# Performance work log

Measured on AMD Instinct MI355X. Metric: run time of the kernel, lower is better.

The kernel has to match this reference:

```python
import jax, jax.numpy as jnp
import numpy as np

B, N = 128, 1024


def setup_inputs() -> dict:
    key = jax.random.key(0)
    k1, k2 = jax.random.split(key)
    vector = jax.random.uniform(k1, (B, N), dtype=jnp.float32)
    interactions = jax.random.normal(k2, (N, N), dtype=jnp.float32)
    return {"vector": vector, "interactions": interactions}


def reference(vector, interactions):
    # x: [B,1,N], y: [B,N,1] -> broadcast dirac delta [B,N,N]
    x = vector[:, None, :]
    y = vector[:, :, None]
    dd = (1.0 - x) * (1.0 - y) + x * y  # [B,N,N]
    dd = jnp.triu(dd)                   # keep upper triangle incl. diagonal
    energy = dd * interactions          # [B,N,N] * [N,N] broadcast
    return energy.reshape(vector.shape[0], -1).sum(axis=1)  # [B]
```

## Files before the change

### kernel.cpp

```cpp
#include <hip/hip_runtime.h>
#include <math.h>

#define NDIM 1024
#define BDIM 128
#define TS 32
#define NT (NDIM / TS)
#define NTILES (NT * (NT + 1) / 2)

__global__ __launch_bounds__(256) void potts_fused(
    const float* __restrict__ V,
    const float* __restrict__ W,
    float* __restrict__ out)
{
    const int t = blockIdx.x;
    const int u = NTILES - 1 - t;
    int kk = (int)(0.5f * (sqrtf((float)(8 * u + 1)) - 1.0f));
    if (kk * (kk + 1) / 2 > u) --kk;
    if ((kk + 1) * (kk + 2) / 2 <= u) ++kk;
    const int ti = NT - 1 - kk;
    const int tj = NT - 1 - (u - kk * (kk + 1) / 2);
    const int I0 = ti * TS, J0 = tj * TS;
    const bool diag = (ti == tj);

    __shared__ float4 vj4[BDIM][8];
    __shared__ float4 vi4[BDIM][8];
    __shared__ float rs[TS];
    __shared__ float red[4][BDIM];

    const int tid = threadIdx.x;
    const int w = tid >> 6;
    const int l = tid & 63;
    const int l7 = l & 7;

    {
        const int r = tid >> 3, c4 = (tid & 7) * 4;
        float4 w4 = *(const float4*)(W + (size_t)(I0 + r) * NDIM + (J0 + c4));
        if (diag) {
            if (c4 + 0 < r) w4.x = 0.0f;
            if (c4 + 1 < r) w4.y = 0.0f;
            if (c4 + 2 < r) w4.z = 0.0f;
            if (c4 + 3 < r) w4.w = 0.0f;
        }
        float rsum = (w4.x + w4.y) + (w4.z + w4.w);
        rsum += __shfl_xor(rsum, 1);
        rsum += __shfl_xor(rsum, 2);
        rsum += __shfl_xor(rsum, 4);
        if ((tid & 7) == 0) rs[r] = rsum;
    }

#pragma unroll
    for (int it = 0; it < 4; ++it) {
        const int fid = tid + 256 * it;
        const int b = fid >> 3, j4 = fid & 7;
        const int g = j4 ^ (b & 7);
        vj4[b][g] = *(const float4*)(V + (size_t)b * NDIM + (J0 + 4 * j4));
        vi4[b][g] = *(const float4*)(V + (size_t)b * NDIM + (I0 + 4 * j4));
    }
    __syncthreads();

    float vj0[TS], vj1[TS];
#pragma unroll
    for (int j4 = 0; j4 < 8; ++j4) {
        const int g = j4 ^ l7;
        const float4 a = vj4[l][g];
        vj0[4*j4+0] = a.x; vj0[4*j4+1] = a.y;
        vj0[4*j4+2] = a.z; vj0[4*j4+3] = a.w;
        const float4 c = vj4[l + 64][g];
        vj1[4*j4+0] = c.x; vj1[4*j4+1] = c.y;
        vj1[4*j4+2] = c.z; vj1[4*j4+3] = c.w;
    }
    float vi0[8], vi1[8];
    {
        const int ga = (2 * w) ^ l7, gb = (2 * w + 1) ^ l7;
        const float4 p  = vi4[l][ga],      q  = vi4[l][gb];
        const float4 p1 = vi4[l + 64][ga], q1 = vi4[l + 64][gb];
        vi0[0]=p.x;  vi0[1]=p.y;  vi0[2]=p.z;  vi0[3]=p.w;
        vi0[4]=q.x;  vi0[5]=q.y;  vi0[6]=q.z;  vi0[7]=q.w;
        vi1[0]=p1.x; vi1[1]=p1.y; vi1[2]=p1.z; vi1[3]=p1.w;
        vi1[4]=q1.x; vi1[5]=q1.y; vi1[6]=q1.z; vi1[7]=q1.w;
    }

    float acc0 = 0.0f, acc1 = 0.0f;
#pragma unroll
    for (int k = 0; k < 8; ++k) {
        const int i = 8 * w + k;
        const float* __restrict__ wrow = W + (size_t)(I0 + i) * NDIM + J0;
        float za0 = 0.f, zb0 = 0.f, za1 = 0.f, zb1 = 0.f;
#pragma unroll
        for (int j4 = 0; j4 < 8; j4 += 2) {
            float4 wa = *(const float4*)(wrow + 4 * j4);
            float4 wb = *(const float4*)(wrow + 4 * j4 + 4);
            if (diag) {
                if (4*j4 + 0 < i) wa.x = 0.0f;
                if (4*j4 + 1 < i) wa.y = 0.0f;
                if (4*j4 + 2 < i) wa.z = 0.0f;
                if (4*j4 + 3 < i) wa.w = 0.0f;
                if (4*j4 + 4 < i) wb.x = 0.0f;
                if (4*j4 + 5 < i) wb.y = 0.0f;
                if (4*j4 + 6 < i) wb.z = 0.0f;
                if (4*j4 + 7 < i) wb.w = 0.0f;
            }
            za0 = fmaf(wa.x, vj0[4*j4+0], za0);
            za0 = fmaf(wa.y, vj0[4*j4+1], za0);
            za0 = fmaf(wa.z, vj0[4*j4+2], za0);
            za0 = fmaf(wa.w, vj0[4*j4+3], za0);
            za1 = fmaf(wa.x, vj1[4*j4+0], za1);
            za1 = fmaf(wa.y, vj1[4*j4+1], za1);
            za1 = fmaf(wa.z, vj1[4*j4+2], za1);
            za1 = fmaf(wa.w, vj1[4*j4+3], za1);
            zb0 = fmaf(wb.x, vj0[4*j4+4], zb0);
            zb0 = fmaf(wb.y, vj0[4*j4+5], zb0);
            zb0 = fmaf(wb.z, vj0[4*j4+6], zb0);
            zb0 = fmaf(wb.w, vj0[4*j4+7], zb0);
            zb1 = fmaf(wb.x, vj1[4*j4+4], zb1);
            zb1 = fmaf(wb.y, vj1[4*j4+5], zb1);
            zb1 = fmaf(wb.z, vj1[4*j4+6], zb1);
            zb1 = fmaf(wb.w, vj1[4*j4+7], zb1);
        }
        const float y0 = vi0[k], y1 = vi1[k];
        const float rsk = rs[i];
        acc0 = fmaf(1.0f - y0, rsk, acc0);
        acc0 = fmaf(2.0f * y0 - 1.0f, za0 + zb0, acc0);
        acc1 = fmaf(1.0f - y1, rsk, acc1);
        acc1 = fmaf(2.0f * y1 - 1.0f, za1 + zb1, acc1);
    }

    red[w][l] = acc0;
    red[w][l + 64] = acc1;
    __syncthreads();
    if (tid < BDIM) {
        const float v4 = (red[0][tid] + red[1][tid]) + (red[2][tid] + red[3][tid]);
        atomicAdd(&out[tid], v4);
    }
}

extern "C" void kernel_launch(void* const* d_in, const int* in_sizes, int n_in,
                              void* d_out, int out_size, void* d_ws, size_t ws_size,
                              hipStream_t stream) {
    const float* V = (const float*)d_in[0];
    const float* W = (const float*)d_in[1];
    float* out = (float*)d_out;
    (void)d_ws; (void)ws_size;

    hipMemsetAsync(d_out, 0, BDIM * sizeof(float), stream);
    potts_fused<<<dim3(NTILES), dim3(256), 0, stream>>>(V, W, out);
}
```

Before: 77.46 us.

## Replace atomic accumulation with per-tile partials and a separate reduction kernel

The main kernel now writes each tile's per-batch sum to a workspace buffer instead of using atomicAdd, and a second kernel reduces the 528 partials per batch row. This also removes the output memset. The V row-slice loads for the i side now go straight from global memory into registers instead of through shared memory, and all global loads are issued up front so their latency overlaps. The cost is an extra kernel launch and a workspace round trip, in exchange for no atomic contention and less shared memory.

```diff
diff --git a/kernel.cpp b/kernel.cpp
--- a/kernel.cpp
+++ b/kernel.cpp
@@ -7,10 +7,10 @@
 #define NT (NDIM / TS)
 #define NTILES (NT * (NT + 1) / 2)
 
-__global__ __launch_bounds__(256) void potts_fused(
+__global__ __launch_bounds__(256) void potts_main(
     const float* __restrict__ V,
     const float* __restrict__ W,
-    float* __restrict__ out)
+    float* __restrict__ partial)
 {
     const int t = blockIdx.x;
     const int u = NTILES - 1 - t;
@@ -23,7 +23,6 @@
     const bool diag = (ti == tj);
 
     __shared__ float4 vj4[BDIM][8];
-    __shared__ float4 vi4[BDIM][8];
     __shared__ float rs[TS];
     __shared__ float red[4][BDIM];
 
@@ -32,15 +31,26 @@
     const int l = tid & 63;
     const int l7 = l & 7;
 
+    const int r = tid >> 3, c4 = (tid & 7) * 4;
+    float4 w4 = *(const float4*)(W + (size_t)(I0 + r) * NDIM + (J0 + c4));
+
+    float4 sv0 = *(const float4*)(V + (size_t)((tid + 0 * 256) >> 3) * NDIM + (J0 + 4 * ((tid + 0 * 256) & 7)));
+    float4 sv1 = *(const float4*)(V + (size_t)((tid + 1 * 256) >> 3) * NDIM + (J0 + 4 * ((tid + 1 * 256) & 7)));
+    float4 sv2 = *(const float4*)(V + (size_t)((tid + 2 * 256) >> 3) * NDIM + (J0 + 4 * ((tid + 2 * 256) & 7)));
+    float4 sv3 = *(const float4*)(V + (size_t)((tid + 3 * 256) >> 3) * NDIM + (J0 + 4 * ((tid + 3 * 256) & 7)));
+
+    const float4 p0 = *(const float4*)(V + (size_t)l * NDIM + (I0 + 8 * w));
+    const float4 q0 = *(const float4*)(V + (size_t)l * NDIM + (I0 + 8 * w + 4));
+    const float4 p1 = *(const float4*)(V + (size_t)(l + 64) * NDIM + (I0 + 8 * w));
+    const float4 q1 = *(const float4*)(V + (size_t)(l + 64) * NDIM + (I0 + 8 * w + 4));
+
+    if (diag) {
+        if (c4 + 0 < r) w4.x = 0.0f;
+        if (c4 + 1 < r) w4.y = 0.0f;
+        if (c4 + 2 < r) w4.z = 0.0f;
+        if (c4 + 3 < r) w4.w = 0.0f;
+    }
     {
-        const int r = tid >> 3, c4 = (tid & 7) * 4;
-        float4 w4 = *(const float4*)(W + (size_t)(I0 + r) * NDIM + (J0 + c4));
-        if (diag) {
-            if (c4 + 0 < r) w4.x = 0.0f;
-            if (c4 + 1 < r) w4.y = 0.0f;
-            if (c4 + 2 < r) w4.z = 0.0f;
-            if (c4 + 3 < r) w4.w = 0.0f;
-        }
         float rsum = (w4.x + w4.y) + (w4.z + w4.w);
         rsum += __shfl_xor(rsum, 1);
         rsum += __shfl_xor(rsum, 2);
@@ -48,13 +58,12 @@
         if ((tid & 7) == 0) rs[r] = rsum;
     }
 
-#pragma unroll
-    for (int it = 0; it < 4; ++it) {
-        const int fid = tid + 256 * it;
-        const int b = fid >> 3, j4 = fid & 7;
-        const int g = j4 ^ (b & 7);
-        vj4[b][g] = *(const float4*)(V + (size_t)b * NDIM + (J0 + 4 * j4));
-        vi4[b][g] = *(const float4*)(V + (size_t)b * NDIM + (I0 + 4 * j4));
+    {
+        int fid, b, j4;
+        fid = tid + 0 * 256; b = fid >> 3; j4 = fid & 7; vj4[b][j4 ^ (b & 7)] = sv0;
+        fid = tid + 1 * 256; b = fid >> 3; j4 = fid & 7; vj4[b][j4 ^ (b & 7)] = sv1;
+        fid = tid + 2 * 256; b = fid >> 3; j4 = fid & 7; vj4[b][j4 ^ (b & 7)] = sv2;
+        fid = tid + 3 * 256; b = fid >> 3; j4 = fid & 7; vj4[b][j4 ^ (b & 7)] = sv3;
     }
     __syncthreads();
 
@@ -70,15 +79,10 @@
         vj1[4*j4+2] = c.z; vj1[4*j4+3] = c.w;
     }
     float vi0[8], vi1[8];
-    {
-        const int ga = (2 * w) ^ l7, gb = (2 * w + 1) ^ l7;
-        const float4 p  = vi4[l][ga],      q  = vi4[l][gb];
-        const float4 p1 = vi4[l + 64][ga], q1 = vi4[l + 64][gb];
-        vi0[0]=p.x;  vi0[1]=p.y;  vi0[2]=p.z;  vi0[3]=p.w;
-        vi0[4]=q.x;  vi0[5]=q.y;  vi0[6]=q.z;  vi0[7]=q.w;
-        vi1[0]=p1.x; vi1[1]=p1.y; vi1[2]=p1.z; vi1[3]=p1.w;
-        vi1[4]=q1.x; vi1[5]=q1.y; vi1[6]=q1.z; vi1[7]=q1.w;
-    }
+    vi0[0]=p0.x; vi0[1]=p0.y; vi0[2]=p0.z; vi0[3]=p0.w;
+    vi0[4]=q0.x; vi0[5]=q0.y; vi0[6]=q0.z; vi0[7]=q0.w;
+    vi1[0]=p1.x; vi1[1]=p1.y; vi1[2]=p1.z; vi1[3]=p1.w;
+    vi1[4]=q1.x; vi1[5]=q1.y; vi1[6]=q1.z; vi1[7]=q1.w;
 
     float acc0 = 0.0f, acc1 = 0.0f;
 #pragma unroll
@@ -129,9 +133,26 @@
     red[w][l + 64] = acc1;
     __syncthreads();
     if (tid < BDIM) {
-        const float v4 = (red[0][tid] + red[1][tid]) + (red[2][tid] + red[3][tid]);
-        atomicAdd(&out[tid], v4);
+        partial[(size_t)tid * NTILES + t] =
+            (red[0][tid] + red[1][tid]) + (red[2][tid] + red[3][tid]);
     }
+}
+
+__global__ __launch_bounds__(256) void potts_red(
+    const float* __restrict__ partial, float* __restrict__ out)
+{
+    const int b = blockIdx.x;
+    const int tid = threadIdx.x;
+    const float* __restrict__ row = partial + (size_t)b * NTILES;
+    float a = row[tid] + row[tid + 256];
+    if (tid < NTILES - 512) a += row[tid + 512];
+#pragma unroll
+    for (int off = 32; off > 0; off >>= 1)
+        a += __shfl_down(a, off);
+    __shared__ float rr[4];
+    if ((tid & 63) == 0) rr[tid >> 6] = a;
+    __syncthreads();
+    if (tid == 0) out[b] = (rr[0] + rr[1]) + (rr[2] + rr[3]);
 }
 
 extern "C" void kernel_launch(void* const* d_in, const int* in_sizes, int n_in,
@@ -140,8 +161,8 @@
     const float* V = (const float*)d_in[0];
     const float* W = (const float*)d_in[1];
     float* out = (float*)d_out;
-    (void)d_ws; (void)ws_size;
+    float* partial = (float*)d_ws;
 
-    hipMemsetAsync(d_out, 0, BDIM * sizeof(float), stream);
-    potts_fused<<<dim3(NTILES), dim3(256), 0, stream>>>(V, W, out);
+    potts_main<<<dim3(NTILES), dim3(256), 0, stream>>>(V, W, partial);
+    potts_red<<<dim3(BDIM), dim3(256), 0, stream>>>(partial, out);
 }
```

Measured after the change: 71.70 us. 7.4% less time.
